# Optimization experiments

Hardware: AMD Instinct MI355X
Metric: run time of the kernel (lower is better)

Reference implementation:

```python
import jax, jax.numpy as jnp
import numpy as np

N_ATOMS = 50000
N_EDGES = 1600000
ATOM_F = 64
NBR_F = 64
RBF = 16


def setup_inputs() -> dict:
    key = jax.random.key(0)
    ks = jax.random.split(key, 12)
    din = 2 * ATOM_F + NBR_F  # input dim to W_1/W_2
    s1 = 1.0 / np.sqrt(din)
    s3 = 1.0 / np.sqrt(NBR_F)
    sr = 1.0 / np.sqrt(RBF)
    return {
        "atom_fea": jax.random.normal(ks[0], (N_ATOMS, ATOM_F), jnp.float32),
        "edge_ij": jax.random.normal(ks[1], (N_EDGES, NBR_F), jnp.float32),
        "nbr_atoms": jax.random.randint(ks[2], (N_EDGES, 2), 0, N_ATOMS),
        "bonds_r": jax.random.normal(ks[3], (N_EDGES, RBF), jnp.float32),
        # params, stored as [in, out] (equivalent to torch Linear W.T)
        "W1": jax.random.uniform(ks[4], (din, NBR_F), jnp.float32, -s1, s1),
        "b1": jax.random.uniform(ks[5], (NBR_F,), jnp.float32, -s1, s1),
        "W2": jax.random.uniform(ks[6], (din, NBR_F), jnp.float32, -s1, s1),
        "b2": jax.random.uniform(ks[7], (NBR_F,), jnp.float32, -s1, s1),
        "Wr": jax.random.uniform(ks[8], (RBF, NBR_F), jnp.float32, -sr, sr),
        "br": jax.random.uniform(ks[9], (NBR_F,), jnp.float32, -sr, sr),
        "W3": jax.random.uniform(ks[10], (NBR_F, NBR_F), jnp.float32, -s3, s3),
        "b3": jax.random.uniform(ks[11], (NBR_F,), jnp.float32, -s3, s3),
    }


def reference(atom_fea, edge_ij, nbr_atoms, bonds_r, W1, b1, W2, b2, Wr, br, W3, b3):
    # gather endpoint atom features and concat with edge features: [E, 2*A+F]
    a_i = atom_fea[nbr_atoms[:, 0]]
    a_j = atom_fea[nbr_atoms[:, 1]]
    x = jnp.concatenate([a_i, a_j, edge_ij], axis=-1)
    # gated MLP edge update
    h = jax.nn.silu(x @ W1 + b1) * jax.nn.sigmoid(x @ W2 + b2)  # [E, F]
    out = jax.nn.silu(h @ W3 + b3) * (bonds_r @ Wr + br)         # [E, F]
    return out
```

## Files before the change

### kernel.cpp

```cpp
#include <hip/hip_runtime.h>
#include <hip/hip_bf16.h>

typedef float    f32x4 __attribute__((ext_vector_type(4)));
typedef short    s16x8 __attribute__((ext_vector_type(8)));
typedef unsigned u32x4 __attribute__((ext_vector_type(4)));

__device__ __forceinline__ unsigned short f2bf(float f) {
    union { __hip_bfloat16 b; unsigned short u; } v;
    v.b = __float2bfloat16(f);
    return v.u;
}
__device__ __forceinline__ unsigned cvtpk(float lo, float hi) {
    unsigned r;
    asm("v_cvt_pk_bf16_f32 %0, %1, %2" : "=v"(r) : "v"(lo), "v"(hi));
    return r;
}
__device__ __forceinline__ float sigf(float x)  {
    return __builtin_amdgcn_rcpf(1.0f + __expf(-x));
}

__device__ __forceinline__ s16x8 pack8(float4 a, float4 b) {
    union { u32x4 u; s16x8 v; } r;
    r.u[0] = cvtpk(a.x, a.y);
    r.u[1] = cvtpk(a.z, a.w);
    r.u[2] = cvtpk(b.x, b.y);
    r.u[3] = cvtpk(b.z, b.w);
    return r.v;
}

__global__ __launch_bounds__(256) void atom_conv_kernel(
    const float* __restrict__ atom_fea, unsigned short* __restrict__ Af, int total)
{
    int i = blockIdx.x * blockDim.x + threadIdx.x;
    const int stride = gridDim.x * blockDim.x;
    for (; i < total; i += stride) {
        int a = i >> 6, p = i & 63;
        int kh = p >> 5, q = (p >> 3) & 3, jj = p & 7;
        int k = kh * 32 + q * 4 + (jj & 3) + ((jj & 4) ? 16 : 0);
        Af[i] = f2bf(atom_fea[(size_t)a * 64 + k]);
    }
}

#define NCH 48

__global__ __launch_bounds__(256, 1) void edge_kernel(
    const unsigned short* __restrict__ Af,
    const float* __restrict__ edge_ij,
    const int*   __restrict__ nbr,
    const float* __restrict__ bonds_r,
    const float* __restrict__ W1, const float* __restrict__ b1,
    const float* __restrict__ W2, const float* __restrict__ b2,
    const float* __restrict__ W3, const float* __restrict__ b3,
    const float* __restrict__ Wr, const float* __restrict__ br,
    float* __restrict__ out, int n_edges)
{
    __shared__ unsigned short wlds[NCH * 512];
    __shared__ float blds[256];

    const int t    = threadIdx.x;
    const int wave = t >> 6;
    const int lane = t & 63;
    const int q    = lane >> 4;
    const int n    = lane & 15;

    for (int ch = 0; ch < NCH; ++ch) {
        int idx = t * 2;
        #pragma unroll
        for (int e2 = 0; e2 < 2; ++e2, ++idx) {
            const int l  = idx >> 3, j = idx & 7;
            const int lq = l >> 4, ln = l & 15;
            const int kk = (j < 4) ? (lq * 4 + j) : (16 + lq * 4 + (j - 4));
            float val;
            if (ch < 24) {
                int kh = ch >> 2, nb = ch & 3;
                val = W1[(size_t)(kh * 32 + kk) * 64 + nb * 16 + ln];
            } else {
                int c2 = ch - 24; int kh = c2 >> 2, nb = c2 & 3;
                val = W2[(size_t)(kh * 32 + kk) * 64 + nb * 16 + ln];
            }
            wlds[ch * 512 + idx] = f2bf(val);
        }
    }
    if (t < 64)        blds[t] = b1[t];
    else if (t < 128)  blds[t] = b2[t - 64];
    else if (t < 192)  blds[t] = b3[t - 128];
    else               blds[t] = br[t - 192];

    s16x8 w3f[8], wrf[4];
    {
        const int ln = lane & 15;
        const int lq = lane >> 4;
        #pragma unroll
        for (int c2 = 0; c2 < 8; ++c2) {
            const int kh = c2 >> 2, nb = c2 & 3;
            s16x8 w;
            #pragma unroll
            for (int j = 0; j < 8; ++j) {
                const int kk = (j < 4) ? (lq * 4 + j) : (16 + lq * 4 + (j - 4));
                w[j] = (short)f2bf(W3[(size_t)(kh * 32 + kk) * 64 + nb * 16 + ln]);
            }
            w3f[c2] = w;
        }
        #pragma unroll
        for (int nb = 0; nb < 4; ++nb) {
            s16x8 w;
            #pragma unroll
            for (int j = 0; j < 8; ++j) {
                const int kk = (j < 4) ? (lq * 4 + j) : (16 + lq * 4 + (j - 4));
                w[j] = (short)(kk < 16 ? f2bf(Wr[(size_t)kk * 64 + nb * 16 + ln]) : 0);
            }
            wrf[nb] = w;
        }
    }
    __syncthreads();

    const int tiles   = (n_edges + 15) >> 4;
    const int tstride = gridDim.x * 4;
    int T = blockIdx.x * 4 + wave;
    if (T >= tiles) return;

    const int2* nb2 = (const int2*)nbr;

    int2 nbc = nb2[min(T * 16 + n, n_edges - 1)];
    int Tn = T + tstride;
    bool havenext = (Tn < tiles);
    int2 nbn = nbc;
    if (havenext) nbn = nb2[min(Tn * 16 + n, n_edges - 1)];

    const int e0 = min(T * 16 + n, n_edges - 1);
    s16x8 ai0 = *(const s16x8*)&Af[(size_t)nbc.x * 64 + q * 8];
    s16x8 ai1 = *(const s16x8*)&Af[(size_t)nbc.x * 64 + 32 + q * 8];
    s16x8 aj0 = *(const s16x8*)&Af[(size_t)nbc.y * 64 + q * 8];
    s16x8 aj1 = *(const s16x8*)&Af[(size_t)nbc.y * 64 + 32 + q * 8];
    const float* xr0 = edge_ij + (size_t)e0 * 64;
    float4 rx0 = *(const float4*)(xr0 +      q * 4);
    float4 rx1 = *(const float4*)(xr0 + 16 + q * 4);
    float4 rx2 = *(const float4*)(xr0 + 32 + q * 4);
    float4 rx3 = *(const float4*)(xr0 + 48 + q * 4);
    float4 rb  = *(const float4*)(bonds_r + (size_t)e0 * 16 + q * 4);

    while (true) {
        const int E0 = T * 16;

        s16x8 xf0 = pack8(rx0, rx1);
        s16x8 xf1 = pack8(rx2, rx3);

        f32x4 acc1[4], acc2[4];
        #pragma unroll
        for (int nb = 0; nb < 4; ++nb) {
            acc1[nb] = *(const f32x4*)&blds[nb * 16 + q * 4];
            acc2[nb] = *(const f32x4*)&blds[64 + nb * 16 + q * 4];
        }

        #pragma unroll
        for (int nb = 0; nb < 4; ++nb) {
            s16x8 w;
            w = *(const s16x8*)&wlds[( 0 + nb) * 512 + lane * 8];
            acc1[nb] = __builtin_amdgcn_mfma_f32_16x16x32_bf16(w, ai0, acc1[nb], 0, 0, 0);
            w = *(const s16x8*)&wlds[( 4 + nb) * 512 + lane * 8];
            acc1[nb] = __builtin_amdgcn_mfma_f32_16x16x32_bf16(w, ai1, acc1[nb], 0, 0, 0);
            w = *(const s16x8*)&wlds[( 8 + nb) * 512 + lane * 8];
            acc1[nb] = __builtin_amdgcn_mfma_f32_16x16x32_bf16(w, aj0, acc1[nb], 0, 0, 0);
            w = *(const s16x8*)&wlds[(12 + nb) * 512 + lane * 8];
            acc1[nb] = __builtin_amdgcn_mfma_f32_16x16x32_bf16(w, aj1, acc1[nb], 0, 0, 0);
            w = *(const s16x8*)&wlds[(24 + nb) * 512 + lane * 8];
            acc2[nb] = __builtin_amdgcn_mfma_f32_16x16x32_bf16(w, ai0, acc2[nb], 0, 0, 0);
            w = *(const s16x8*)&wlds[(28 + nb) * 512 + lane * 8];
            acc2[nb] = __builtin_amdgcn_mfma_f32_16x16x32_bf16(w, ai1, acc2[nb], 0, 0, 0);
            w = *(const s16x8*)&wlds[(32 + nb) * 512 + lane * 8];
            acc2[nb] = __builtin_amdgcn_mfma_f32_16x16x32_bf16(w, aj0, acc2[nb], 0, 0, 0);
            w = *(const s16x8*)&wlds[(36 + nb) * 512 + lane * 8];
            acc2[nb] = __builtin_amdgcn_mfma_f32_16x16x32_bf16(w, aj1, acc2[nb], 0, 0, 0);
        }

        s16x8 nai0 = ai0, nai1 = ai1, naj0 = aj0, naj1 = aj1;
        float4 nrx0 = rx0, nrx1 = rx1, nrx2 = rx2, nrx3 = rx3, nrb = rb;
        if (havenext) {
            const int ne = min(Tn * 16 + n, n_edges - 1);
            nai0 = *(const s16x8*)&Af[(size_t)nbn.x * 64 + q * 8];
            nai1 = *(const s16x8*)&Af[(size_t)nbn.x * 64 + 32 + q * 8];
            naj0 = *(const s16x8*)&Af[(size_t)nbn.y * 64 + q * 8];
            naj1 = *(const s16x8*)&Af[(size_t)nbn.y * 64 + 32 + q * 8];
            const float* nxr = edge_ij + (size_t)ne * 64;
            nrx0 = *(const float4*)(nxr +      q * 4);
            nrx1 = *(const float4*)(nxr + 16 + q * 4);
            nrx2 = *(const float4*)(nxr + 32 + q * 4);
            nrx3 = *(const float4*)(nxr + 48 + q * 4);
            nrb  = *(const float4*)(bonds_r + (size_t)ne * 16 + q * 4);
            const int T2 = Tn + tstride;
            if (T2 < tiles) nbn = nb2[min(T2 * 16 + n, n_edges - 1)];
        }

        #pragma unroll
        for (int nb = 0; nb < 4; ++nb) {
            s16x8 w;
            w = *(const s16x8*)&wlds[(16 + nb) * 512 + lane * 8];
            acc1[nb] = __builtin_amdgcn_mfma_f32_16x16x32_bf16(w, xf0, acc1[nb], 0, 0, 0);
            w = *(const s16x8*)&wlds[(20 + nb) * 512 + lane * 8];
            acc1[nb] = __builtin_amdgcn_mfma_f32_16x16x32_bf16(w, xf1, acc1[nb], 0, 0, 0);
            w = *(const s16x8*)&wlds[(40 + nb) * 512 + lane * 8];
            acc2[nb] = __builtin_amdgcn_mfma_f32_16x16x32_bf16(w, xf0, acc2[nb], 0, 0, 0);
            w = *(const s16x8*)&wlds[(44 + nb) * 512 + lane * 8];
            acc2[nb] = __builtin_amdgcn_mfma_f32_16x16x32_bf16(w, xf1, acc2[nb], 0, 0, 0);
        }

        s16x8 bfrag;
        {
            union { u32x4 u; s16x8 v; } B;
            B.u[0] = cvtpk(rb.x, rb.y);
            B.u[1] = cvtpk(rb.z, rb.w);
            B.u[2] = 0; B.u[3] = 0;
            bfrag = B.v;
        }

        f32x4 h[4];
        #pragma unroll
        for (int nb = 0; nb < 4; ++nb) {
            f32x4 s1 = acc1[nb], s2 = acc2[nb], hv;
            #pragma unroll
            for (int j = 0; j < 4; ++j)
                hv[j] = s1[j] * sigf(s1[j]) * sigf(s2[j]);
            h[nb] = hv;
        }
        s16x8 hf0, hf1;
        {
            union { u32x4 u; s16x8 v; } H0, H1;
            H0.u[0] = cvtpk(h[0][0], h[0][1]);
            H0.u[1] = cvtpk(h[0][2], h[0][3]);
            H0.u[2] = cvtpk(h[1][0], h[1][1]);
            H0.u[3] = cvtpk(h[1][2], h[1][3]);
            H1.u[0] = cvtpk(h[2][0], h[2][1]);
            H1.u[1] = cvtpk(h[2][2], h[2][3]);
            H1.u[2] = cvtpk(h[3][0], h[3][1]);
            H1.u[3] = cvtpk(h[3][2], h[3][3]);
            hf0 = H0.v; hf1 = H1.v;
        }

        f32x4 a3[4], g[4];
        #pragma unroll
        for (int nb = 0; nb < 4; ++nb) { a3[nb] = (f32x4){0,0,0,0}; g[nb] = (f32x4){0,0,0,0}; }
        #pragma unroll
        for (int nb = 0; nb < 4; ++nb) {
            a3[nb] = __builtin_amdgcn_mfma_f32_16x16x32_bf16(hf0, w3f[nb],     a3[nb], 0, 0, 0);
            a3[nb] = __builtin_amdgcn_mfma_f32_16x16x32_bf16(hf1, w3f[4 + nb], a3[nb], 0, 0, 0);
            g[nb]  = __builtin_amdgcn_mfma_f32_16x16x32_bf16(bfrag, wrf[nb],   g[nb],  0, 0, 0);
        }

        float* outp = out + (size_t)(E0 + q * 4) * 64 + n;
        if (E0 + 16 <= n_edges) {
            #pragma unroll
            for (int nb = 0; nb < 4; ++nb) {
                const float b3s = blds[128 + nb * 16 + n];
                const float brs = blds[192 + nb * 16 + n];
                f32x4 s  = a3[nb] + b3s;
                f32x4 gg = g[nb] + brs;
                f32x4 o;
                #pragma unroll
                for (int j = 0; j < 4; ++j)
                    o[j] = s[j] * sigf(s[j]) * gg[j];
                #pragma unroll
                for (int j = 0; j < 4; ++j)
                    outp[j * 64 + nb * 16] = o[j];
            }
        } else {
            #pragma unroll
            for (int nb = 0; nb < 4; ++nb) {
                const float b3s = blds[128 + nb * 16 + n];
                const float brs = blds[192 + nb * 16 + n];
                f32x4 s  = a3[nb] + b3s;
                f32x4 gg = g[nb] + brs;
                #pragma unroll
                for (int j = 0; j < 4; ++j)
                    if (E0 + q * 4 + j < n_edges)
                        outp[j * 64 + nb * 16] = s[j] * sigf(s[j]) * gg[j];
            }
        }

        if (!havenext) break;
        T = Tn;
        Tn = T + tstride;
        havenext = (Tn < tiles);
        ai0 = nai0; ai1 = nai1; aj0 = naj0; aj1 = naj1;
        rx0 = nrx0; rx1 = nrx1; rx2 = nrx2; rx3 = nrx3; rb = nrb;
    }
}

extern "C" void kernel_launch(void* const* d_in, const int* in_sizes, int n_in,
                              void* d_out, int out_size, void* d_ws, size_t ws_size,
                              hipStream_t stream) {
    const float* atom_fea = (const float*)d_in[0];
    const float* edge_ij  = (const float*)d_in[1];
    const int*   nbr      = (const int*)  d_in[2];
    const float* bonds_r  = (const float*)d_in[3];
    const float* W1 = (const float*)d_in[4];
    const float* b1 = (const float*)d_in[5];
    const float* W2 = (const float*)d_in[6];
    const float* b2 = (const float*)d_in[7];
    const float* Wr = (const float*)d_in[8];
    const float* br = (const float*)d_in[9];
    const float* W3 = (const float*)d_in[10];
    const float* b3 = (const float*)d_in[11];
    float* out = (float*)d_out;
    unsigned short* Af = (unsigned short*)d_ws;

    const int n_atoms = in_sizes[0] / 64;
    const int n_edges = in_sizes[2] / 2;

    hipLaunchKernelGGL(atom_conv_kernel, dim3(2048), dim3(256), 0, stream,
                       atom_fea, Af, n_atoms * 64);

    hipLaunchKernelGGL(edge_kernel, dim3(1024), dim3(256), 0, stream,
                       Af, edge_ij, nbr, bonds_r,
                       W1, b1, W2, b2, W3, b3, Wr, br, out, n_edges);
}
```

Baseline: 256.0 us.

## Process two 16-edge tiles per wave iteration to widen the prefetch window

Each wave now handles a pair of 16-edge tiles (32 edges) per loop iteration. The gathers and loads for both tiles of the next pair are issued while layer-1 MFMAs run, which doubles the bytes in flight per wave and spreads each global load's latency over more compute. The code is refactored into inline helpers and the prefetch now writes straight into the current registers. The cost is roughly double the register footprint for inputs and accumulators, which could cause spills at one block per CU, and the grid stride now covers half as many iterations.

```diff
diff --git a/kernel.cpp b/kernel.cpp
--- a/kernel.cpp
+++ b/kernel.cpp
@@ -38,6 +38,126 @@
         int kh = p >> 5, q = (p >> 3) & 3, jj = p & 7;
         int k = kh * 32 + q * 4 + (jj & 3) + ((jj & 4) ? 16 : 0);
         Af[i] = f2bf(atom_fea[(size_t)a * 64 + k]);
+    }
+}
+
+__device__ __forceinline__ void layer1_atom(
+    const unsigned short* wlds, int lane,
+    s16x8 ai0, s16x8 ai1, s16x8 aj0, s16x8 aj1,
+    f32x4 acc1[4], f32x4 acc2[4])
+{
+    #pragma unroll
+    for (int nb = 0; nb < 4; ++nb) {
+        s16x8 w;
+        w = *(const s16x8*)&wlds[( 0 + nb) * 512 + lane * 8];
+        acc1[nb] = __builtin_amdgcn_mfma_f32_16x16x32_bf16(w, ai0, acc1[nb], 0, 0, 0);
+        w = *(const s16x8*)&wlds[( 4 + nb) * 512 + lane * 8];
+        acc1[nb] = __builtin_amdgcn_mfma_f32_16x16x32_bf16(w, ai1, acc1[nb], 0, 0, 0);
+        w = *(const s16x8*)&wlds[( 8 + nb) * 512 + lane * 8];
+        acc1[nb] = __builtin_amdgcn_mfma_f32_16x16x32_bf16(w, aj0, acc1[nb], 0, 0, 0);
+        w = *(const s16x8*)&wlds[(12 + nb) * 512 + lane * 8];
+        acc1[nb] = __builtin_amdgcn_mfma_f32_16x16x32_bf16(w, aj1, acc1[nb], 0, 0, 0);
+        w = *(const s16x8*)&wlds[(24 + nb) * 512 + lane * 8];
+        acc2[nb] = __builtin_amdgcn_mfma_f32_16x16x32_bf16(w, ai0, acc2[nb], 0, 0, 0);
+        w = *(const s16x8*)&wlds[(28 + nb) * 512 + lane * 8];
+        acc2[nb] = __builtin_amdgcn_mfma_f32_16x16x32_bf16(w, ai1, acc2[nb], 0, 0, 0);
+        w = *(const s16x8*)&wlds[(32 + nb) * 512 + lane * 8];
+        acc2[nb] = __builtin_amdgcn_mfma_f32_16x16x32_bf16(w, aj0, acc2[nb], 0, 0, 0);
+        w = *(const s16x8*)&wlds[(36 + nb) * 512 + lane * 8];
+        acc2[nb] = __builtin_amdgcn_mfma_f32_16x16x32_bf16(w, aj1, acc2[nb], 0, 0, 0);
+    }
+}
+
+__device__ __forceinline__ void layer1_eij(
+    const unsigned short* wlds, int lane,
+    s16x8 xf0, s16x8 xf1, f32x4 acc1[4], f32x4 acc2[4])
+{
+    #pragma unroll
+    for (int nb = 0; nb < 4; ++nb) {
+        s16x8 w;
+        w = *(const s16x8*)&wlds[(16 + nb) * 512 + lane * 8];
+        acc1[nb] = __builtin_amdgcn_mfma_f32_16x16x32_bf16(w, xf0, acc1[nb], 0, 0, 0);
+        w = *(const s16x8*)&wlds[(20 + nb) * 512 + lane * 8];
+        acc1[nb] = __builtin_amdgcn_mfma_f32_16x16x32_bf16(w, xf1, acc1[nb], 0, 0, 0);
+        w = *(const s16x8*)&wlds[(40 + nb) * 512 + lane * 8];
+        acc2[nb] = __builtin_amdgcn_mfma_f32_16x16x32_bf16(w, xf0, acc2[nb], 0, 0, 0);
+        w = *(const s16x8*)&wlds[(44 + nb) * 512 + lane * 8];
+        acc2[nb] = __builtin_amdgcn_mfma_f32_16x16x32_bf16(w, xf1, acc2[nb], 0, 0, 0);
+    }
+}
+
+__device__ __forceinline__ void finish_tile(
+    f32x4 acc1[4], f32x4 acc2[4], float4 rb,
+    const s16x8 w3f[8], const s16x8 wrf[4], const float* blds,
+    float* __restrict__ out, int row0, int n_edges, int q, int n)
+{
+    s16x8 bfrag;
+    {
+        union { u32x4 u; s16x8 v; } B;
+        B.u[0] = cvtpk(rb.x, rb.y);
+        B.u[1] = cvtpk(rb.z, rb.w);
+        B.u[2] = 0; B.u[3] = 0;
+        bfrag = B.v;
+    }
+    f32x4 h[4];
+    #pragma unroll
+    for (int nb = 0; nb < 4; ++nb) {
+        f32x4 s1 = acc1[nb], s2 = acc2[nb], hv;
+        #pragma unroll
+        for (int j = 0; j < 4; ++j)
+            hv[j] = s1[j] * sigf(s1[j]) * sigf(s2[j]);
+        h[nb] = hv;
+    }
+    s16x8 hf0, hf1;
+    {
+        union { u32x4 u; s16x8 v; } H0, H1;
+        H0.u[0] = cvtpk(h[0][0], h[0][1]);
+        H0.u[1] = cvtpk(h[0][2], h[0][3]);
+        H0.u[2] = cvtpk(h[1][0], h[1][1]);
+        H0.u[3] = cvtpk(h[1][2], h[1][3]);
+        H1.u[0] = cvtpk(h[2][0], h[2][1]);
+        H1.u[1] = cvtpk(h[2][2], h[2][3]);
+        H1.u[2] = cvtpk(h[3][0], h[3][1]);
+        H1.u[3] = cvtpk(h[3][2], h[3][3]);
+        hf0 = H0.v; hf1 = H1.v;
+    }
+    f32x4 a3[4], g[4];
+    #pragma unroll
+    for (int nb = 0; nb < 4; ++nb) { a3[nb] = (f32x4){0,0,0,0}; g[nb] = (f32x4){0,0,0,0}; }
+    #pragma unroll
+    for (int nb = 0; nb < 4; ++nb) {
+        a3[nb] = __builtin_amdgcn_mfma_f32_16x16x32_bf16(hf0, w3f[nb],     a3[nb], 0, 0, 0);
+        a3[nb] = __builtin_amdgcn_mfma_f32_16x16x32_bf16(hf1, w3f[4 + nb], a3[nb], 0, 0, 0);
+        g[nb]  = __builtin_amdgcn_mfma_f32_16x16x32_bf16(bfrag, wrf[nb],   g[nb],  0, 0, 0);
+    }
+    float* outp = out + (size_t)(row0 + q * 4) * 64 + n;
+    if (row0 + 16 <= n_edges) {
+        #pragma unroll
+        for (int nb = 0; nb < 4; ++nb) {
+            const float b3s = blds[128 + nb * 16 + n];
+            const float brs = blds[192 + nb * 16 + n];
+            f32x4 s  = a3[nb] + b3s;
+            f32x4 gg = g[nb] + brs;
+            f32x4 o;
+            #pragma unroll
+            for (int j = 0; j < 4; ++j)
+                o[j] = s[j] * sigf(s[j]) * gg[j];
+            #pragma unroll
+            for (int j = 0; j < 4; ++j)
+                outp[j * 64 + nb * 16] = o[j];
+        }
+    } else {
+        #pragma unroll
+        for (int nb = 0; nb < 4; ++nb) {
+            const float b3s = blds[128 + nb * 16 + n];
+            const float brs = blds[192 + nb * 16 + n];
+            f32x4 s  = a3[nb] + b3s;
+            f32x4 gg = g[nb] + brs;
+            #pragma unroll
+            for (int j = 0; j < 4; ++j)
+                if (row0 + q * 4 + j < n_edges)
+                    outp[j * 64 + nb * 16] = s[j] * sigf(s[j]) * gg[j];
+        }
     }
 }
 
@@ -114,174 +234,108 @@
     }
     __syncthreads();
 
-    const int tiles   = (n_edges + 15) >> 4;
+    const int pairs   = (n_edges + 31) >> 5;
     const int tstride = gridDim.x * 4;
-    int T = blockIdx.x * 4 + wave;
-    if (T >= tiles) return;
+    int P = blockIdx.x * 4 + wave;
+    if (P >= pairs) return;
 
     const int2* nb2 = (const int2*)nbr;
 
-    int2 nbc = nb2[min(T * 16 + n, n_edges - 1)];
-    int Tn = T + tstride;
-    bool havenext = (Tn < tiles);
-    int2 nbn = nbc;
-    if (havenext) nbn = nb2[min(Tn * 16 + n, n_edges - 1)];
-
-    const int e0 = min(T * 16 + n, n_edges - 1);
-    s16x8 ai0 = *(const s16x8*)&Af[(size_t)nbc.x * 64 + q * 8];
-    s16x8 ai1 = *(const s16x8*)&Af[(size_t)nbc.x * 64 + 32 + q * 8];
-    s16x8 aj0 = *(const s16x8*)&Af[(size_t)nbc.y * 64 + q * 8];
-    s16x8 aj1 = *(const s16x8*)&Af[(size_t)nbc.y * 64 + 32 + q * 8];
-    const float* xr0 = edge_ij + (size_t)e0 * 64;
-    float4 rx0 = *(const float4*)(xr0 +      q * 4);
-    float4 rx1 = *(const float4*)(xr0 + 16 + q * 4);
-    float4 rx2 = *(const float4*)(xr0 + 32 + q * 4);
-    float4 rx3 = *(const float4*)(xr0 + 48 + q * 4);
-    float4 rb  = *(const float4*)(bonds_r + (size_t)e0 * 16 + q * 4);
+    int2 nbcA = nb2[min(P * 32 + n,      n_edges - 1)];
+    int2 nbcB = nb2[min(P * 32 + 16 + n, n_edges - 1)];
+    int Pn = P + tstride;
+    bool havenext = (Pn < pairs);
+    int2 nbnA = nbcA, nbnB = nbcB;
+    if (havenext) {
+        nbnA = nb2[min(Pn * 32 + n,      n_edges - 1)];
+        nbnB = nb2[min(Pn * 32 + 16 + n, n_edges - 1)];
+    }
+
+    const int eA = min(P * 32 + n,      n_edges - 1);
+    const int eB = min(P * 32 + 16 + n, n_edges - 1);
+    s16x8 aiA0 = *(const s16x8*)&Af[(size_t)nbcA.x * 64 + q * 8];
+    s16x8 aiA1 = *(const s16x8*)&Af[(size_t)nbcA.x * 64 + 32 + q * 8];
+    s16x8 ajA0 = *(const s16x8*)&Af[(size_t)nbcA.y * 64 + q * 8];
+    s16x8 ajA1 = *(const s16x8*)&Af[(size_t)nbcA.y * 64 + 32 + q * 8];
+    s16x8 aiB0 = *(const s16x8*)&Af[(size_t)nbcB.x * 64 + q * 8];
+    s16x8 aiB1 = *(const s16x8*)&Af[(size_t)nbcB.x * 64 + 32 + q * 8];
+    s16x8 ajB0 = *(const s16x8*)&Af[(size_t)nbcB.y * 64 + q * 8];
+    s16x8 ajB1 = *(const s16x8*)&Af[(size_t)nbcB.y * 64 + 32 + q * 8];
+    const float* xrA = edge_ij + (size_t)eA * 64;
+    const float* xrB = edge_ij + (size_t)eB * 64;
+    float4 rxA0 = *(const float4*)(xrA +      q * 4);
+    float4 rxA1 = *(const float4*)(xrA + 16 + q * 4);
+    float4 rxA2 = *(const float4*)(xrA + 32 + q * 4);
+    float4 rxA3 = *(const float4*)(xrA + 48 + q * 4);
+    float4 rxB0 = *(const float4*)(xrB +      q * 4);
+    float4 rxB1 = *(const float4*)(xrB + 16 + q * 4);
+    float4 rxB2 = *(const float4*)(xrB + 32 + q * 4);
+    float4 rxB3 = *(const float4*)(xrB + 48 + q * 4);
+    float4 rbA  = *(const float4*)(bonds_r + (size_t)eA * 16 + q * 4);
+    float4 rbB  = *(const float4*)(bonds_r + (size_t)eB * 16 + q * 4);
 
     while (true) {
-        const int E0 = T * 16;
-
-        s16x8 xf0 = pack8(rx0, rx1);
-        s16x8 xf1 = pack8(rx2, rx3);
-
-        f32x4 acc1[4], acc2[4];
+        const int E0 = P * 32;
+
+        s16x8 xfA0 = pack8(rxA0, rxA1);
+        s16x8 xfA1 = pack8(rxA2, rxA3);
+        s16x8 xfB0 = pack8(rxB0, rxB1);
+        s16x8 xfB1 = pack8(rxB2, rxB3);
+
+        f32x4 acc1A[4], acc2A[4], acc1B[4], acc2B[4];
         #pragma unroll
         for (int nb = 0; nb < 4; ++nb) {
-            acc1[nb] = *(const f32x4*)&blds[nb * 16 + q * 4];
-            acc2[nb] = *(const f32x4*)&blds[64 + nb * 16 + q * 4];
-        }
-
-        #pragma unroll
-        for (int nb = 0; nb < 4; ++nb) {
-            s16x8 w;
-            w = *(const s16x8*)&wlds[( 0 + nb) * 512 + lane * 8];
-            acc1[nb] = __builtin_amdgcn_mfma_f32_16x16x32_bf16(w, ai0, acc1[nb], 0, 0, 0);
-            w = *(const s16x8*)&wlds[( 4 + nb) * 512 + lane * 8];
-            acc1[nb] = __builtin_amdgcn_mfma_f32_16x16x32_bf16(w, ai1, acc1[nb], 0, 0, 0);
-            w = *(const s16x8*)&wlds[( 8 + nb) * 512 + lane * 8];
-            acc1[nb] = __builtin_amdgcn_mfma_f32_16x16x32_bf16(w, aj0, acc1[nb], 0, 0, 0);
-            w = *(const s16x8*)&wlds[(12 + nb) * 512 + lane * 8];
-            acc1[nb] = __builtin_amdgcn_mfma_f32_16x16x32_bf16(w, aj1, acc1[nb], 0, 0, 0);
-            w = *(const s16x8*)&wlds[(24 + nb) * 512 + lane * 8];
-            acc2[nb] = __builtin_amdgcn_mfma_f32_16x16x32_bf16(w, ai0, acc2[nb], 0, 0, 0);
-            w = *(const s16x8*)&wlds[(28 + nb) * 512 + lane * 8];
-            acc2[nb] = __builtin_amdgcn_mfma_f32_16x16x32_bf16(w, ai1, acc2[nb], 0, 0, 0);
-            w = *(const s16x8*)&wlds[(32 + nb) * 512 + lane * 8];
-            acc2[nb] = __builtin_amdgcn_mfma_f32_16x16x32_bf16(w, aj0, acc2[nb], 0, 0, 0);
-            w = *(const s16x8*)&wlds[(36 + nb) * 512 + lane * 8];
-            acc2[nb] = __builtin_amdgcn_mfma_f32_16x16x32_bf16(w, aj1, acc2[nb], 0, 0, 0);
-        }
-
-        s16x8 nai0 = ai0, nai1 = ai1, naj0 = aj0, naj1 = aj1;
-        float4 nrx0 = rx0, nrx1 = rx1, nrx2 = rx2, nrx3 = rx3, nrb = rb;
+            acc1A[nb] = *(const f32x4*)&blds[nb * 16 + q * 4];
+            acc2A[nb] = *(const f32x4*)&blds[64 + nb * 16 + q * 4];
+            acc1B[nb] = acc1A[nb];
+            acc2B[nb] = acc2A[nb];
+        }
+        layer1_atom(wlds, lane, aiA0, aiA1, ajA0, ajA1, acc1A, acc2A);
+        layer1_atom(wlds, lane, aiB0, aiB1, ajB0, ajB1, acc1B, acc2B);
+
         if (havenext) {
-            const int ne = min(Tn * 16 + n, n_edges - 1);
-            nai0 = *(const s16x8*)&Af[(size_t)nbn.x * 64 + q * 8];
-            nai1 = *(const s16x8*)&Af[(size_t)nbn.x * 64 + 32 + q * 8];
-            naj0 = *(const s16x8*)&Af[(size_t)nbn.y * 64 + q * 8];
-            naj1 = *(const s16x8*)&Af[(size_t)nbn.y * 64 + 32 + q * 8];
-            const float* nxr = edge_ij + (size_t)ne * 64;
-            nrx0 = *(const float4*)(nxr +      q * 4);
-            nrx1 = *(const float4*)(nxr + 16 + q * 4);
-            nrx2 = *(const float4*)(nxr + 32 + q * 4);
-            nrx3 = *(const float4*)(nxr + 48 + q * 4);
-            nrb  = *(const float4*)(bonds_r + (size_t)ne * 16 + q * 4);
-            const int T2 = Tn + tstride;
-            if (T2 < tiles) nbn = nb2[min(T2 * 16 + n, n_edges - 1)];
-        }
-
-        #pragma unroll
-        for (int nb = 0; nb < 4; ++nb) {
-            s16x8 w;
-            w = *(const s16x8*)&wlds[(16 + nb) * 512 + lane * 8];
-            acc1[nb] = __builtin_amdgcn_mfma_f32_16x16x32_bf16(w, xf0, acc1[nb], 0, 0, 0);
-            w = *(const s16x8*)&wlds[(20 + nb) * 512 + lane * 8];
-            acc1[nb] = __builtin_amdgcn_mfma_f32_16x16x32_bf16(w, xf1, acc1[nb], 0, 0, 0);
-            w = *(const s16x8*)&wlds[(40 + nb) * 512 + lane * 8];
-            acc2[nb] = __builtin_amdgcn_mfma_f32_16x16x32_bf16(w, xf0, acc2[nb], 0, 0, 0);
-            w = *(const s16x8*)&wlds[(44 + nb) * 512 + lane * 8];
-            acc2[nb] = __builtin_amdgcn_mfma_f32_16x16x32_bf16(w, xf1, acc2[nb], 0, 0, 0);
-        }
-
-        s16x8 bfrag;
-        {
-            union { u32x4 u; s16x8 v; } B;
-            B.u[0] = cvtpk(rb.x, rb.y);
-            B.u[1] = cvtpk(rb.z, rb.w);
-            B.u[2] = 0; B.u[3] = 0;
-            bfrag = B.v;
-        }
-
-        f32x4 h[4];
-        #pragma unroll
-        for (int nb = 0; nb < 4; ++nb) {
-            f32x4 s1 = acc1[nb], s2 = acc2[nb], hv;
-            #pragma unroll
-            for (int j = 0; j < 4; ++j)
-                hv[j] = s1[j] * sigf(s1[j]) * sigf(s2[j]);
-            h[nb] = hv;
-        }
-        s16x8 hf0, hf1;
-        {
-            union { u32x4 u; s16x8 v; } H0, H1;
-            H0.u[0] = cvtpk(h[0][0], h[0][1]);
-            H0.u[1] = cvtpk(h[0][2], h[0][3]);
-            H0.u[2] = cvtpk(h[1][0], h[1][1]);
-            H0.u[3] = cvtpk(h[1][2], h[1][3]);
-            H1.u[0] = cvtpk(h[2][0], h[2][1]);
-            H1.u[1] = cvtpk(h[2][2], h[2][3]);
-            H1.u[2] = cvtpk(h[3][0], h[3][1]);
-            H1.u[3] = cvtpk(h[3][2], h[3][3]);
-            hf0 = H0.v; hf1 = H1.v;
-        }
-
-        f32x4 a3[4], g[4];
-        #pragma unroll
-        for (int nb = 0; nb < 4; ++nb) { a3[nb] = (f32x4){0,0,0,0}; g[nb] = (f32x4){0,0,0,0}; }
-        #pragma unroll
-        for (int nb = 0; nb < 4; ++nb) {
-            a3[nb] = __builtin_amdgcn_mfma_f32_16x16x32_bf16(hf0, w3f[nb],     a3[nb], 0, 0, 0);
-            a3[nb] = __builtin_amdgcn_mfma_f32_16x16x32_bf16(hf1, w3f[4 + nb], a3[nb], 0, 0, 0);
-            g[nb]  = __builtin_amdgcn_mfma_f32_16x16x32_bf16(bfrag, wrf[nb],   g[nb],  0, 0, 0);
-        }
-
-        float* outp = out + (size_t)(E0 + q * 4) * 64 + n;
-        if (E0 + 16 <= n_edges) {
-            #pragma unroll
-            for (int nb = 0; nb < 4; ++nb) {
-                const float b3s = blds[128 + nb * 16 + n];
-                const float brs = blds[192 + nb * 16 + n];
-                f32x4 s  = a3[nb] + b3s;
-                f32x4 gg = g[nb] + brs;
-                f32x4 o;
-                #pragma unroll
-                for (int j = 0; j < 4; ++j)
-                    o[j] = s[j] * sigf(s[j]) * gg[j];
-                #pragma unroll
-                for (int j = 0; j < 4; ++j)
-                    outp[j * 64 + nb * 16] = o[j];
+            const int neA = min(Pn * 32 + n,      n_edges - 1);
+            const int neB = min(Pn * 32 + 16 + n, n_edges - 1);
+            aiA0 = *(const s16x8*)&Af[(size_t)nbnA.x * 64 + q * 8];
+            aiA1 = *(const s16x8*)&Af[(size_t)nbnA.x * 64 + 32 + q * 8];
+            ajA0 = *(const s16x8*)&Af[(size_t)nbnA.y * 64 + q * 8];
+            ajA1 = *(const s16x8*)&Af[(size_t)nbnA.y * 64 + 32 + q * 8];
+            aiB0 = *(const s16x8*)&Af[(size_t)nbnB.x * 64 + q * 8];
+            aiB1 = *(const s16x8*)&Af[(size_t)nbnB.x * 64 + 32 + q * 8];
+            ajB0 = *(const s16x8*)&Af[(size_t)nbnB.y * 64 + q * 8];
+            ajB1 = *(const s16x8*)&Af[(size_t)nbnB.y * 64 + 32 + q * 8];
+            const float* nxrA = edge_ij + (size_t)neA * 64;
+            const float* nxrB = edge_ij + (size_t)neB * 64;
+            rxA0 = *(const float4*)(nxrA +      q * 4);
+            rxA1 = *(const float4*)(nxrA + 16 + q * 4);
+            rxA2 = *(const float4*)(nxrA + 32 + q * 4);
+            rxA3 = *(const float4*)(nxrA + 48 + q * 4);
+            rxB0 = *(const float4*)(nxrB +      q * 4);
+            rxB1 = *(const float4*)(nxrB + 16 + q * 4);
+            rxB2 = *(const float4*)(nxrB + 32 + q * 4);
+            rxB3 = *(const float4*)(nxrB + 48 + q * 4);
+            const float4 trbA = *(const float4*)(bonds_r + (size_t)neA * 16 + q * 4);
+            const float4 trbB = *(const float4*)(bonds_r + (size_t)neB * 16 + q * 4);
+            const int P2 = Pn + tstride;
+            if (P2 < pairs) {
+                nbnA = nb2[min(P2 * 32 + n,      n_edges - 1)];
+                nbnB = nb2[min(P2 * 32 + 16 + n, n_edges - 1)];
             }
+            layer1_eij(wlds, lane, xfA0, xfA1, acc1A, acc2A);
+            finish_tile(acc1A, acc2A, rbA, w3f, wrf, blds, out, E0, n_edges, q, n);
+            layer1_eij(wlds, lane, xfB0, xfB1, acc1B, acc2B);
+            finish_tile(acc1B, acc2B, rbB, w3f, wrf, blds, out, E0 + 16, n_edges, q, n);
+            rbA = trbA; rbB = trbB;
+            P = Pn;
+            Pn = P + tstride;
+            havenext = (Pn < pairs);
         } else {
-            #pragma unroll
-            for (int nb = 0; nb < 4; ++nb) {
-                const float b3s = blds[128 + nb * 16 + n];
-                const float brs = blds[192 + nb * 16 + n];
-                f32x4 s  = a3[nb] + b3s;
-                f32x4 gg = g[nb] + brs;
-                #pragma unroll
-                for (int j = 0; j < 4; ++j)
-                    if (E0 + q * 4 + j < n_edges)
-                        outp[j * 64 + nb * 16] = s[j] * sigf(s[j]) * gg[j];
-            }
-        }
-
-        if (!havenext) break;
-        T = Tn;
-        Tn = T + tstride;
-        havenext = (Tn < tiles);
-        ai0 = nai0; ai1 = nai1; aj0 = naj0; aj1 = naj1;
-        rx0 = nrx0; rx1 = nrx1; rx2 = nrx2; rx3 = nrx3; rb = nrb;
+            layer1_eij(wlds, lane, xfA0, xfA1, acc1A, acc2A);
+            finish_tile(acc1A, acc2A, rbA, w3f, wrf, blds, out, E0, n_edges, q, n);
+            layer1_eij(wlds, lane, xfB0, xfB1, acc1B, acc2B);
+            finish_tile(acc1B, acc2B, rbB, w3f, wrf, blds, out, E0 + 16, n_edges, q, n);
+            break;
+        }
     }
 }
 
```

Result: slower. 280.1 us (+9.4%).
